# Kernel optimization log

Hardware: AMD Instinct MI355X
Metric: run time of the kernel (lower is better)

## Reference

```python
import jax, jax.numpy as jnp
import numpy as np

H = 256   # hidden size
E = 128   # embedding dim per step
C = 512   # context dim (640 - 128)
V = 32000 # vocab
T = 20
B = 128


def _lstm_seq(x_seq, h0, Wih, Whh, bih, bhh):
    """Run LSTMCell over time. NOTE: faithful to the original bug — the cell
    state passed in every step is the initial zeros (updated c is discarded)."""
    c0 = jnp.zeros_like(h0)
    xg = jnp.einsum('tbe,ge->tbg', x_seq, Wih) + bih  # precompute input gates [T,B,4H]

    def step(h, xg_t):
        g = xg_t + h @ Whh.T + bhh
        i, f, gg, o = jnp.split(g, 4, axis=-1)
        c_new = jax.nn.sigmoid(f) * c0 + jax.nn.sigmoid(i) * jnp.tanh(gg)
        h_new = jax.nn.sigmoid(o) * jnp.tanh(c_new)
        return h_new, h_new

    _, hs = jax.lax.scan(step, h0, xg)
    return hs  # [T,B,H]


def setup_inputs() -> dict:
    key = jax.random.key(0)
    ks = jax.random.split(key, 16)
    s = 0.05
    inp = {
        'inputPrev': jax.random.normal(ks[0], (T, B, E), jnp.float32),
        'inputNext': jax.random.normal(ks[1], (T, B, E), jnp.float32),
        'context':   jax.random.normal(ks[2], (B, C), jnp.float32),
        'hidden1':   jax.random.normal(ks[3], (1, H), jnp.float32) * s,
        'hidden2':   jax.random.normal(ks[4], (1, H), jnp.float32) * s,
        'Wih_p': jax.random.normal(ks[5], (4 * H, E + C), jnp.float32) * s,
        'Whh_p': jax.random.normal(ks[6], (4 * H, H), jnp.float32) * s,
        'bih_p': jax.random.normal(ks[7], (4 * H,), jnp.float32) * s,
        'bhh_p': jax.random.normal(ks[8], (4 * H,), jnp.float32) * s,
        'Wih_n': jax.random.normal(ks[9], (4 * H, E + C), jnp.float32) * s,
        'Whh_n': jax.random.normal(ks[10], (4 * H, H), jnp.float32) * s,
        'bih_n': jax.random.normal(ks[11], (4 * H,), jnp.float32) * s,
        'bhh_n': jax.random.normal(ks[12], (4 * H,), jnp.float32) * s,
        'Wp': jax.random.normal(ks[13], (V, H), jnp.float32) * s,
        'bp': jax.random.normal(ks[14], (V,), jnp.float32) * s,
    }
    return inp


def reference(inputPrev, inputNext, context, hidden1, hidden2,
              Wih_p, Whh_p, bih_p, bhh_p,
              Wih_n, Whh_n, bih_n, bhh_n, Wp, bp):
    ctx = jnp.broadcast_to(context, (T, B, C))
    x_prev = jnp.concatenate([inputPrev, ctx], axis=-1)  # [T,B,640]
    x_next = jnp.concatenate([inputNext, ctx], axis=-1)

    h10 = jnp.broadcast_to(hidden1, (B, H))
    h20 = jnp.broadcast_to(hidden2, (B, H))

    hs_prev = _lstm_seq(x_prev, h10, Wih_p, Whh_p, bih_p, bhh_p)  # [T,B,H]
    hs_next = _lstm_seq(x_next, h20, Wih_n, Whh_n, bih_n, bhh_n)

    logits_prev = jnp.einsum('tbh,vh->tbv', hs_prev, Wp) + bp
    logits_next = jnp.einsum('tbh,vh->tbv', hs_next, Wp) + bp
    return (logits_prev, logits_next)
```

## Files before the change

### kernel.cpp

```cpp
#include <hip/hip_runtime.h>
#include <cstdint>
#include <cstddef>

#define T_STEPS 20
#define B_SZ 128
#define H_SZ 256
#define E_SZ 128
#define C_SZ 512
#define V_SZ 32000
#define G3H 768

typedef __bf16 bf16x8 __attribute__((ext_vector_type(8)));
typedef float f32x4 __attribute__((ext_vector_type(4)));
typedef unsigned short u16x8 __attribute__((ext_vector_type(8)));

#define AS1 __attribute__((address_space(1)))
#define AS3 __attribute__((address_space(3)))

__device__ __forceinline__ unsigned short f2bf(float f) {
  unsigned int u = __builtin_bit_cast(unsigned int, f);
  u += 0x7fffu + ((u >> 16) & 1u);
  return (unsigned short)(u >> 16);
}

__global__ void k_zero(int* __restrict__ c) {
  if (threadIdx.x < 64) c[threadIdx.x] = 0;
}

__global__ __launch_bounds__(256) void k_prep(const float* __restrict__ Whh_p,
    const float* __restrict__ Whh_n, const float* __restrict__ h1, const float* __restrict__ h2,
    unsigned short* __restrict__ whh_bs, unsigned short* __restrict__ hsb) {
  const int idx = blockIdx.x * 256 + threadIdx.x;
  const int NW = 2 * 16 * 48 * 256;
  if (idx < NW) {
    const int k = idx & 255;
    const int n = (idx >> 8) % 48;
    const int tt = ((idx >> 8) / 48) & 15;
    const int l = idx / (16 * 48 * 256);
    const int gate = n >> 4;
    const int c = n & 15;
    const int row = (gate == 0 ? 0 : (gate == 1 ? 512 : 768)) + tt * 16 + c;
    const int ksrc = (k & 7) | (((k >> 3) ^ (n & 7)) << 3);
    const float* W = l ? Whh_n : Whh_p;
    whh_bs[idx] = f2bf(W[(size_t)row * 256 + ksrc]);
  } else {
    const int i2 = idx - NW;
    const int k = i2 & 255;
    const int b = (i2 >> 8) & 127;
    const int l = i2 >> 15;
    const int ksrc = (k & 7) | (((k >> 3) ^ (b & 7)) << 3);
    const float* h = l ? h2 : h1;
    hsb[(size_t)(l * 21) * 32768 + (size_t)b * 256 + k] = f2bf(h[ksrc]);
  }
}

__global__ __launch_bounds__(256) void k_ctx_gemm(const float* __restrict__ context,
    const float* __restrict__ Wih_p, const float* __restrict__ Wih_n,
    const float* __restrict__ bih_p, const float* __restrict__ bhh_p,
    const float* __restrict__ bih_n, const float* __restrict__ bhh_n,
    float* __restrict__ ctxg) {
  const int bid = blockIdx.x;
  const int l = bid / 48;
  const int bt = (bid / 3) & 15;
  const int gt = bid % 3;
  const int b0 = bt * 8;
  const int g = gt * 256 + threadIdx.x;
  const int row = g + (gt > 0 ? 256 : 0);
  __shared__ float csh[8][C_SZ];
  for (int i = threadIdx.x; i < 8 * C_SZ; i += 256)
    csh[i >> 9][i & 511] = context[(size_t)(b0 + (i >> 9)) * C_SZ + (i & 511)];
  __syncthreads();
  const float* W = (l ? Wih_n : Wih_p) + (size_t)row * 640 + E_SZ;
  float acc[8] = {};
  for (int c = 0; c < C_SZ; c += 4) {
    const float4 w = *(const float4*)(W + c);
#pragma unroll
    for (int bb = 0; bb < 8; ++bb) {
      const float4 h = *(const float4*)(&csh[bb][c]);
      acc[bb] += w.x * h.x + w.y * h.y + w.z * h.z + w.w * h.w;
    }
  }
  const float bias = l ? (bih_n[row] + bhh_n[row]) : (bih_p[row] + bhh_p[row]);
#pragma unroll
  for (int bb = 0; bb < 8; ++bb)
    ctxg[((size_t)l * B_SZ + b0 + bb) * G3H + g] = acc[bb] + bias;
}

__global__ __launch_bounds__(256) void k_in_gemm(const float* __restrict__ inP,
    const float* __restrict__ inN,
    const float* __restrict__ Wih_p, const float* __restrict__ Wih_n,
    const float* __restrict__ ctxg, float* __restrict__ xg) {
  const int bid = blockIdx.x;
  const int l = bid / 480;
  const int rest = bid % 480;
  const int rt = rest / 3;
  const int gt = rest % 3;
  const int r0 = rt * 16;
  const int g = gt * 256 + threadIdx.x;
  const int row = g + (gt > 0 ? 256 : 0);
  __shared__ float ish[16][E_SZ];
  const float* inp = l ? inN : inP;
  for (int i = threadIdx.x; i < 16 * E_SZ; i += 256)
    ish[i >> 7][i & 127] = inp[(size_t)(r0 + (i >> 7)) * E_SZ + (i & 127)];
  __syncthreads();
  const float* W = (l ? Wih_n : Wih_p) + (size_t)row * 640;
  float acc[16] = {};
  for (int k = 0; k < E_SZ; k += 4) {
    const float4 w = *(const float4*)(W + k);
#pragma unroll
    for (int rr = 0; rr < 16; ++rr) {
      const float4 h = *(const float4*)(&ish[rr][k]);
      acc[rr] += w.x * h.x + w.y * h.y + w.z * h.z + w.w * h.w;
    }
  }
#pragma unroll
  for (int rr = 0; rr < 16; ++rr) {
    const int b = (r0 + rr) & 127;
    const float cv = ctxg[((size_t)l * B_SZ + b) * G3H + g];
    xg[((size_t)l * (T_STEPS * B_SZ) + r0 + rr) * G3H + g] = acc[rr] + cv;
  }
}

__global__ __launch_bounds__(256, 1) void k_steps(const unsigned short* __restrict__ hsb_in,
    const unsigned short* __restrict__ whh_bs, const float* __restrict__ xg,
    unsigned short* __restrict__ hsb, int* __restrict__ cnt) {
  __shared__ unsigned short wls[48 * 256];
  __shared__ unsigned short hls[128 * 256];
  __shared__ float xls[128 * 3 * 16];
  const int tid = threadIdx.x;
  const int lane = tid & 63;
  const int wave = tid >> 6;
  const int l = blockIdx.x >> 4;
  const int tt = blockIdx.x & 15;

  {
    const unsigned short* wsrc = whh_bs + (size_t)(l * 16 + tt) * 12288 + tid * 8;
#pragma unroll
    for (int i = 0; i < 6; ++i)
      __builtin_amdgcn_global_load_lds((const AS1 void*)(wsrc + i * 2048),
                                       (AS3 void*)(wls + tid * 8 + i * 2048), 16, 0, 0);
  }

  for (int t = 0; t < T_STEPS; ++t) {
    const unsigned short* hsrc = hsb_in + (size_t)(l * 21 + t) * 32768 + tid * 8;
#pragma unroll
    for (int i = 0; i < 16; ++i)
      __builtin_amdgcn_global_load_lds((const AS1 void*)(hsrc + i * 2048),
                                       (AS3 void*)(hls + tid * 8 + i * 2048), 16, 0, 0);
    const size_t xgbase = ((size_t)(l * T_STEPS + t) * B_SZ) * G3H;
#pragma unroll
    for (int i = 0; i < 6; ++i) {
      const int q = tid + i * 256;
      const int b = q / 12;
      const int r = q - b * 12;
      const int gate = r >> 2;
      const int cg = r & 3;
      const float* src = xg + xgbase + (size_t)b * G3H + gate * 256 + tt * 16 + cg * 4;
      __builtin_amdgcn_global_load_lds((const AS1 void*)src,
                                       (AS3 void*)((char*)xls + q * 16), 16, 0, 0);
    }
    asm volatile("s_waitcnt vmcnt(0)" ::: "memory");
    __builtin_amdgcn_s_barrier();

    f32x4 acc[2][3] = {};
#pragma unroll
    for (int kf = 0; kf < 8; ++kf) {
      const int ch = kf * 4 + (lane >> 4);
      bf16x8 bf[3];
#pragma unroll
      for (int nt = 0; nt < 3; ++nt) {
        const int n = nt * 16 + (lane & 15);
        bf[nt] = __builtin_bit_cast(bf16x8, *(const u16x8*)(wls + n * 256 + ((ch ^ (n & 7)) << 3)));
      }
#pragma unroll
      for (int m = 0; m < 2; ++m) {
        const int b = wave * 32 + m * 16 + (lane & 15);
        const bf16x8 af = __builtin_bit_cast(bf16x8, *(const u16x8*)(hls + b * 256 + ((ch ^ (b & 7)) << 3)));
#pragma unroll
        for (int nt = 0; nt < 3; ++nt)
          acc[m][nt] = __builtin_amdgcn_mfma_f32_16x16x32_bf16(af, bf[nt], acc[m][nt], 0, 0, 0);
      }
    }

    unsigned short* hout = hsb + (size_t)(l * 21 + 1 + t) * 32768;
#pragma unroll
    for (int m = 0; m < 2; ++m) {
#pragma unroll
      for (int i = 0; i < 4; ++i) {
        const int b = wave * 32 + m * 16 + (lane >> 4) * 4 + i;
        const int col = lane & 15;
        const float gi = xls[(b * 3 + 0) * 16 + col] + acc[m][0][i];
        const float gg = xls[(b * 3 + 1) * 16 + col] + acc[m][1][i];
        const float go = xls[(b * 3 + 2) * 16 + col] + acc[m][2][i];
        const float c = (1.0f / (1.0f + expf(-gi))) * tanhf(gg);
        const float h = (1.0f / (1.0f + expf(-go))) * tanhf(c);
        const int j = tt * 16 + col;
        const int kpos = (j & 7) | (((j >> 3) ^ (b & 7)) << 3);
        hout[(size_t)b * 256 + kpos] = f2bf(h);
      }
    }

    if (t < T_STEPS - 1) {
      asm volatile("s_waitcnt vmcnt(0)" ::: "memory");
      __syncthreads();
      if (tid == 0) {
        __hip_atomic_fetch_add(&cnt[l * T_STEPS + t], 1, __ATOMIC_RELEASE, __HIP_MEMORY_SCOPE_AGENT);
        while (__hip_atomic_load(&cnt[l * T_STEPS + t], __ATOMIC_RELAXED, __HIP_MEMORY_SCOPE_AGENT) < 16)
          __builtin_amdgcn_s_sleep(1);
      }
      __syncthreads();
      __builtin_amdgcn_fence(__ATOMIC_ACQUIRE, "agent");
    }
  }
}

__global__ __launch_bounds__(256, 2) void k_proj(const unsigned short* __restrict__ hsb,
    const float* __restrict__ Wp, const float* __restrict__ bias, float* __restrict__ out) {
  __shared__ unsigned short smem[3 * 32 * 256];
  const int tid = threadIdx.x;
  const int lane = tid & 63;
  const int wave = tid >> 6;
  const int wgrp = wave >> 1;
  const int wc = wave & 1;
  const int n_base = blockIdx.x * 64 + wc * 32;
  bf16x8 bfr[2][8];
#pragma unroll
  for (int nt = 0; nt < 2; ++nt) {
    const int n_g = n_base + nt * 16 + (lane & 15);
    const float* src = Wp + (size_t)n_g * 256 + (lane >> 4) * 8;
#pragma unroll
    for (int kf = 0; kf < 8; ++kf) {
      const float4 a = *(const float4*)(src + kf * 32);
      const float4 b = *(const float4*)(src + kf * 32 + 4);
      u16x8 u;
      u[0] = f2bf(a.x); u[1] = f2bf(a.y); u[2] = f2bf(a.z); u[3] = f2bf(a.w);
      u[4] = f2bf(b.x); u[5] = f2bf(b.y); u[6] = f2bf(b.z); u[7] = f2bf(b.w);
      bfr[nt][kf] = __builtin_bit_cast(bf16x8, u);
    }
  }
  const float bv0 = bias[n_base + (lane & 15)];
  const float bv1 = bias[n_base + 16 + (lane & 15)];

#define STAGE_A(IT, BUF)                                                                   \
  {                                                                                        \
    const int it_ = (IT);                                                                  \
    const int l_ = it_ >= 80;                                                              \
    const int t_ = (it_ - l_ * 80) >> 2;                                                   \
    const int b0_ = (it_ & 3) * 32;                                                        \
    const unsigned short* src_ = hsb + (size_t)(l_ * 21 + 1 + t_) * 32768 + b0_ * 256 + tid * 8; \
    unsigned short* dst_ = smem + (BUF) * 8192 + tid * 8;                                  \
    _Pragma("unroll")                                                                      \
    for (int i_ = 0; i_ < 4; ++i_)                                                         \
      __builtin_amdgcn_global_load_lds((const AS1 void*)(src_ + i_ * 2048),                \
                                       (AS3 void*)(dst_ + i_ * 2048), 16, 0, 0);           \
  }

  STAGE_A(0, 0);
  STAGE_A(1, 1);
  const int lr = wgrp * 16 + (lane & 15);
  for (int it = 0; it < 160; ++it) {
    __builtin_amdgcn_s_barrier();
    if (it + 2 < 160) STAGE_A(it + 2, (it + 2) % 3);
    if (it == 0) { asm volatile("s_waitcnt vmcnt(8)" ::: "memory"); }
    else         { asm volatile("s_waitcnt vmcnt(16)" ::: "memory"); }
    __builtin_amdgcn_s_barrier();
    const unsigned short* sA = smem + (it % 3) * 8192;
    f32x4 acc0 = {}, acc1 = {};
#pragma unroll
    for (int kf = 0; kf < 8; ++kf) {
      const int ch = (kf * 4 + (lane >> 4)) ^ (lr & 7);
      const bf16x8 af = __builtin_bit_cast(bf16x8, *(const u16x8*)(sA + lr * 256 + (ch << 3)));
      acc0 = __builtin_amdgcn_mfma_f32_16x16x32_bf16(af, bfr[0][kf], acc0, 0, 0, 0);
      acc1 = __builtin_amdgcn_mfma_f32_16x16x32_bf16(af, bfr[1][kf], acc1, 0, 0, 0);
    }
    const size_t row0 = (size_t)it * 32 + wgrp * 16 + (lane >> 4) * 4;
    float* o0 = out + row0 * V_SZ + n_base + (lane & 15);
#pragma unroll
    for (int i = 0; i < 4; ++i) {
      __builtin_nontemporal_store(acc0[i] + bv0, &o0[(size_t)i * V_SZ]);
      __builtin_nontemporal_store(acc1[i] + bv1, &o0[(size_t)i * V_SZ + 16]);
    }
  }
#undef STAGE_A
}

extern "C" void kernel_launch(void* const* d_in, const int* in_sizes, int n_in,
                              void* d_out, int out_size, void* d_ws, size_t ws_size,
                              hipStream_t stream) {
  (void)in_sizes; (void)n_in; (void)out_size; (void)ws_size;
  const float* inputPrev = (const float*)d_in[0];
  const float* inputNext = (const float*)d_in[1];
  const float* context   = (const float*)d_in[2];
  const float* hidden1   = (const float*)d_in[3];
  const float* hidden2   = (const float*)d_in[4];
  const float* Wih_p = (const float*)d_in[5];
  const float* Whh_p = (const float*)d_in[6];
  const float* bih_p = (const float*)d_in[7];
  const float* bhh_p = (const float*)d_in[8];
  const float* Wih_n = (const float*)d_in[9];
  const float* Whh_n = (const float*)d_in[10];
  const float* bih_n = (const float*)d_in[11];
  const float* bhh_n = (const float*)d_in[12];
  const float* Wp = (const float*)d_in[13];
  const float* bp = (const float*)d_in[14];
  float* out = (float*)d_out;

  char* ws = (char*)d_ws;
  float* xg_all        = (float*)(ws + 0);
  float* ctxg          = (float*)(ws + 15728640);
  unsigned short* hsb  = (unsigned short*)(ws + 16515072);
  unsigned short* whhb = (unsigned short*)(ws + 19267584);
  int* cnt             = (int*)(ws + 20054016);

  k_zero<<<1, 64, 0, stream>>>(cnt);
  k_prep<<<1792, 256, 0, stream>>>(Whh_p, Whh_n, hidden1, hidden2, whhb, hsb);
  k_ctx_gemm<<<96, 256, 0, stream>>>(context, Wih_p, Wih_n, bih_p, bhh_p, bih_n, bhh_n, ctxg);
  k_in_gemm<<<960, 256, 0, stream>>>(inputPrev, inputNext, Wih_p, Wih_n, ctxg, xg_all);
  k_steps<<<32, 256, 0, stream>>>(hsb, whhb, xg_all, hsb, cnt);
  k_proj<<<500, 256, 0, stream>>>(hsb, Wp, bp, out);
}
```

Baseline: 372.0 us.

## Partition LSTM recurrence by batch to remove cross-block grid synchronization

The recurrent step kernel is re-partitioned so that each block owns 16 batch rows and all 768 gate columns, instead of 16 gate columns across all 128 batch rows. Each block keeps its hidden state in LDS, which removes the per-step global atomic barrier across 16 blocks and the per-step reload of the full hidden state. The cost is that the whole recurrent weight matrix is streamed from global/L2 through a double-buffered LDS pipeline every step, and only 16 blocks run. The initial hidden broadcast moves into the step kernel, and the counter-zeroing kernel is dropped.

```diff
diff --git a/kernel.cpp b/kernel.cpp
--- a/kernel.cpp
+++ b/kernel.cpp
@@ -23,35 +23,18 @@
   return (unsigned short)(u >> 16);
 }
 
-__global__ void k_zero(int* __restrict__ c) {
-  if (threadIdx.x < 64) c[threadIdx.x] = 0;
-}
-
 __global__ __launch_bounds__(256) void k_prep(const float* __restrict__ Whh_p,
-    const float* __restrict__ Whh_n, const float* __restrict__ h1, const float* __restrict__ h2,
-    unsigned short* __restrict__ whh_bs, unsigned short* __restrict__ hsb) {
+    const float* __restrict__ Whh_n, unsigned short* __restrict__ whh_bs) {
   const int idx = blockIdx.x * 256 + threadIdx.x;
-  const int NW = 2 * 16 * 48 * 256;
-  if (idx < NW) {
-    const int k = idx & 255;
-    const int n = (idx >> 8) % 48;
-    const int tt = ((idx >> 8) / 48) & 15;
-    const int l = idx / (16 * 48 * 256);
-    const int gate = n >> 4;
-    const int c = n & 15;
-    const int row = (gate == 0 ? 0 : (gate == 1 ? 512 : 768)) + tt * 16 + c;
-    const int ksrc = (k & 7) | (((k >> 3) ^ (n & 7)) << 3);
-    const float* W = l ? Whh_n : Whh_p;
-    whh_bs[idx] = f2bf(W[(size_t)row * 256 + ksrc]);
-  } else {
-    const int i2 = idx - NW;
-    const int k = i2 & 255;
-    const int b = (i2 >> 8) & 127;
-    const int l = i2 >> 15;
-    const int ksrc = (k & 7) | (((k >> 3) ^ (b & 7)) << 3);
-    const float* h = l ? h2 : h1;
-    hsb[(size_t)(l * 21) * 32768 + (size_t)b * 256 + k] = f2bf(h[ksrc]);
-  }
+  const int k = idx & 255;
+  const int r = (idx >> 8) % 768;
+  const int l = idx / (768 * 256);
+  const int gate = r >> 8;
+  const int col = r & 255;
+  const int row = (gate == 0 ? 0 : (gate == 1 ? 512 : 768)) + col;
+  const int ksrc = (k & 7) | (((k >> 3) ^ (r & 7)) << 3);
+  const float* W = l ? Whh_n : Whh_p;
+  whh_bs[idx] = f2bf(W[(size_t)row * 256 + ksrc]);
 }
 
 __global__ __launch_bounds__(256) void k_ctx_gemm(const float* __restrict__ context,
@@ -121,97 +104,109 @@
   }
 }
 
-__global__ __launch_bounds__(256, 1) void k_steps(const unsigned short* __restrict__ hsb_in,
-    const unsigned short* __restrict__ whh_bs, const float* __restrict__ xg,
-    unsigned short* __restrict__ hsb, int* __restrict__ cnt) {
-  __shared__ unsigned short wls[48 * 256];
-  __shared__ unsigned short hls[128 * 256];
-  __shared__ float xls[128 * 3 * 16];
+__global__ __launch_bounds__(256, 1) void k_steps(const unsigned short* __restrict__ whh_bs,
+    const float* __restrict__ xg, const float* __restrict__ h1, const float* __restrict__ h2,
+    unsigned short* __restrict__ hsb) {
+  __shared__ unsigned short buf[2][64 * 256];
+  __shared__ unsigned short hls[16 * 256];
   const int tid = threadIdx.x;
   const int lane = tid & 63;
   const int wave = tid >> 6;
-  const int l = blockIdx.x >> 4;
-  const int tt = blockIdx.x & 15;
+  const int l = blockIdx.x >> 3;
+  const int bt = blockIdx.x & 7;
 
   {
-    const unsigned short* wsrc = whh_bs + (size_t)(l * 16 + tt) * 12288 + tid * 8;
-#pragma unroll
-    for (int i = 0; i < 6; ++i)
-      __builtin_amdgcn_global_load_lds((const AS1 void*)(wsrc + i * 2048),
-                                       (AS3 void*)(wls + tid * 8 + i * 2048), 16, 0, 0);
+    const float* h0src = l ? h2 : h1;
+    const unsigned short hb = f2bf(h0src[tid]);
+    const int klo = tid & 7, khi = tid >> 3;
+#pragma unroll
+    for (int b = 0; b < 16; ++b)
+      hls[b * 256 + ((((khi) ^ (b & 7)) << 3) | klo)] = hb;
+  }
+  __syncthreads();
+
+  const unsigned short* wbase = whh_bs + (size_t)l * 768 * 256;
+  const int jn = wave * 16 + (lane & 15);
+  const int bloc = (lane >> 4) * 4;
+
+#define STAGE_W(C, BUF)                                                                  \
+  {                                                                                      \
+    const unsigned short* src_ = wbase + (size_t)(C) * 64 * 256 + tid * 8;               \
+    unsigned short* dst_ = (unsigned short*)buf[(BUF)] + tid * 8;                        \
+    _Pragma("unroll")                                                                    \
+    for (int i_ = 0; i_ < 8; ++i_)                                                       \
+      __builtin_amdgcn_global_load_lds((const AS1 void*)(src_ + i_ * 2048),              \
+                                       (AS3 void*)(dst_ + i_ * 2048), 16, 0, 0);         \
   }
 
   for (int t = 0; t < T_STEPS; ++t) {
-    const unsigned short* hsrc = hsb_in + (size_t)(l * 21 + t) * 32768 + tid * 8;
-#pragma unroll
-    for (int i = 0; i < 16; ++i)
-      __builtin_amdgcn_global_load_lds((const AS1 void*)(hsrc + i * 2048),
-                                       (AS3 void*)(hls + tid * 8 + i * 2048), 16, 0, 0);
-    const size_t xgbase = ((size_t)(l * T_STEPS + t) * B_SZ) * G3H;
-#pragma unroll
-    for (int i = 0; i < 6; ++i) {
-      const int q = tid + i * 256;
-      const int b = q / 12;
-      const int r = q - b * 12;
-      const int gate = r >> 2;
-      const int cg = r & 3;
-      const float* src = xg + xgbase + (size_t)b * G3H + gate * 256 + tt * 16 + cg * 4;
-      __builtin_amdgcn_global_load_lds((const AS1 void*)src,
-                                       (AS3 void*)((char*)xls + q * 16), 16, 0, 0);
-    }
-    asm volatile("s_waitcnt vmcnt(0)" ::: "memory");
-    __builtin_amdgcn_s_barrier();
-
-    f32x4 acc[2][3] = {};
-#pragma unroll
-    for (int kf = 0; kf < 8; ++kf) {
-      const int ch = kf * 4 + (lane >> 4);
-      bf16x8 bf[3];
-#pragma unroll
-      for (int nt = 0; nt < 3; ++nt) {
-        const int n = nt * 16 + (lane & 15);
-        bf[nt] = __builtin_bit_cast(bf16x8, *(const u16x8*)(wls + n * 256 + ((ch ^ (n & 7)) << 3)));
+    float xgv[3][4][4];
+    {
+      const float* xrow = xg + ((size_t)(l * T_STEPS + t) * B_SZ + bt * 16 + bloc) * G3H;
+#pragma unroll
+      for (int gate = 0; gate < 3; ++gate)
+#pragma unroll
+        for (int cg = 0; cg < 4; ++cg)
+#pragma unroll
+          for (int ii = 0; ii < 3 + 1; ++ii)
+            xgv[gate][cg][ii] = xrow[(size_t)ii * G3H + gate * 256 + cg * 64 + jn];
+    }
+    bf16x8 af[8];
+    {
+      const int b = lane & 15;
+#pragma unroll
+      for (int kf = 0; kf < 8; ++kf) {
+        const int ch = kf * 4 + (lane >> 4);
+        af[kf] = __builtin_bit_cast(bf16x8, *(const u16x8*)(hls + b * 256 + ((ch ^ (b & 7)) << 3)));
       }
-#pragma unroll
-      for (int m = 0; m < 2; ++m) {
-        const int b = wave * 32 + m * 16 + (lane & 15);
-        const bf16x8 af = __builtin_bit_cast(bf16x8, *(const u16x8*)(hls + b * 256 + ((ch ^ (b & 7)) << 3)));
-#pragma unroll
-        for (int nt = 0; nt < 3; ++nt)
-          acc[m][nt] = __builtin_amdgcn_mfma_f32_16x16x32_bf16(af, bf[nt], acc[m][nt], 0, 0, 0);
+    }
+
+    f32x4 acc[12];
+#pragma unroll
+    for (int c = 0; c < 12; ++c) acc[c] = f32x4{0.f, 0.f, 0.f, 0.f};
+
+    STAGE_W(0, 0);
+#pragma unroll
+    for (int c = 0; c < 12; ++c) {
+      if (c < 11) {
+        STAGE_W(c + 1, (c + 1) & 1);
+        asm volatile("s_waitcnt vmcnt(8)" ::: "memory");
+      } else {
+        asm volatile("s_waitcnt vmcnt(0)" ::: "memory");
       }
-    }
-
-    unsigned short* hout = hsb + (size_t)(l * 21 + 1 + t) * 32768;
-#pragma unroll
-    for (int m = 0; m < 2; ++m) {
-#pragma unroll
-      for (int i = 0; i < 4; ++i) {
-        const int b = wave * 32 + m * 16 + (lane >> 4) * 4 + i;
-        const int col = lane & 15;
-        const float gi = xls[(b * 3 + 0) * 16 + col] + acc[m][0][i];
-        const float gg = xls[(b * 3 + 1) * 16 + col] + acc[m][1][i];
-        const float go = xls[(b * 3 + 2) * 16 + col] + acc[m][2][i];
-        const float c = (1.0f / (1.0f + expf(-gi))) * tanhf(gg);
-        const float h = (1.0f / (1.0f + expf(-go))) * tanhf(c);
-        const int j = tt * 16 + col;
+      __builtin_amdgcn_s_barrier();
+      const unsigned short* wb = (const unsigned short*)buf[c & 1];
+#pragma unroll
+      for (int kf = 0; kf < 8; ++kf) {
+        const int ch = kf * 4 + (lane >> 4);
+        const bf16x8 bfv = __builtin_bit_cast(bf16x8,
+            *(const u16x8*)(wb + jn * 256 + ((ch ^ (jn & 7)) << 3)));
+        acc[c] = __builtin_amdgcn_mfma_f32_16x16x32_bf16(af[kf], bfv, acc[c], 0, 0, 0);
+      }
+      __builtin_amdgcn_s_barrier();
+    }
+
+    unsigned short* hout = hsb + (size_t)(l * T_STEPS + t) * 32768;
+#pragma unroll
+    for (int cg = 0; cg < 4; ++cg) {
+      const int j = cg * 64 + jn;
+#pragma unroll
+      for (int ii = 0; ii < 4; ++ii) {
+        const int b = bloc + ii;
+        const float gi = xgv[0][cg][ii] + acc[cg][ii];
+        const float gg = xgv[1][cg][ii] + acc[4 + cg][ii];
+        const float go = xgv[2][cg][ii] + acc[8 + cg][ii];
+        const float cc = (1.0f / (1.0f + expf(-gi))) * tanhf(gg);
+        const float h = (1.0f / (1.0f + expf(-go))) * tanhf(cc);
+        const unsigned short hb = f2bf(h);
         const int kpos = (j & 7) | (((j >> 3) ^ (b & 7)) << 3);
-        hout[(size_t)b * 256 + kpos] = f2bf(h);
+        hout[(size_t)(bt * 16 + b) * 256 + kpos] = hb;
+        hls[b * 256 + kpos] = hb;
       }
     }
-
-    if (t < T_STEPS - 1) {
-      asm volatile("s_waitcnt vmcnt(0)" ::: "memory");
-      __syncthreads();
-      if (tid == 0) {
-        __hip_atomic_fetch_add(&cnt[l * T_STEPS + t], 1, __ATOMIC_RELEASE, __HIP_MEMORY_SCOPE_AGENT);
-        while (__hip_atomic_load(&cnt[l * T_STEPS + t], __ATOMIC_RELAXED, __HIP_MEMORY_SCOPE_AGENT) < 16)
-          __builtin_amdgcn_s_sleep(1);
-      }
-      __syncthreads();
-      __builtin_amdgcn_fence(__ATOMIC_ACQUIRE, "agent");
-    }
-  }
+    __syncthreads();
+  }
+#undef STAGE_W
 }
 
 __global__ __launch_bounds__(256, 2) void k_proj(const unsigned short* __restrict__ hsb,
@@ -247,7 +242,7 @@
     const int l_ = it_ >= 80;                                                              \
     const int t_ = (it_ - l_ * 80) >> 2;                                                   \
     const int b0_ = (it_ & 3) * 32;                                                        \
-    const unsigned short* src_ = hsb + (size_t)(l_ * 21 + 1 + t_) * 32768 + b0_ * 256 + tid * 8; \
+    const unsigned short* src_ = hsb + (size_t)(l_ * T_STEPS + t_) * 32768 + b0_ * 256 + tid * 8; \
     unsigned short* dst_ = smem + (BUF) * 8192 + tid * 8;                                  \
     _Pragma("unroll")                                                                      \
     for (int i_ = 0; i_ < 4; ++i_)                                                         \
@@ -309,13 +304,11 @@
   float* xg_all        = (float*)(ws + 0);
   float* ctxg          = (float*)(ws + 15728640);
   unsigned short* hsb  = (unsigned short*)(ws + 16515072);
-  unsigned short* whhb = (unsigned short*)(ws + 19267584);
-  int* cnt             = (int*)(ws + 20054016);
-
-  k_zero<<<1, 64, 0, stream>>>(cnt);
-  k_prep<<<1792, 256, 0, stream>>>(Whh_p, Whh_n, hidden1, hidden2, whhb, hsb);
+  unsigned short* whhb = (unsigned short*)(ws + 19136512);
+
+  k_prep<<<1536, 256, 0, stream>>>(Whh_p, Whh_n, whhb);
   k_ctx_gemm<<<96, 256, 0, stream>>>(context, Wih_p, Wih_n, bih_p, bhh_p, bih_n, bhh_n, ctxg);
   k_in_gemm<<<960, 256, 0, stream>>>(inputPrev, inputNext, Wih_p, Wih_n, ctxg, xg_all);
-  k_steps<<<32, 256, 0, stream>>>(hsb, whhb, xg_all, hsb, cnt);
+  k_steps<<<16, 256, 0, stream>>>(whhb, xg_all, hidden1, hidden2, hsb);
   k_proj<<<500, 256, 0, stream>>>(hsb, Wp, bp, out);
 }
```

Measured after the change: 450.6 us. 1.21x slower.

## Fuse recurrent steps and vocab projection into one persistent kernel with dataflow waits

Applied to the files above, without the earlier changes.

Merges the recurrent-step kernel and the output projection into one persistent kernel of 256 blocks. The first 32 blocks run the LSTM steps and publish per-step counters. All blocks then take vocab strips from an atomic ticket queue. Before staging each hidden-state tile, the projection waits on that step's counter, so projection of early timesteps overlaps the later recurrent steps. The aim is to hide the projection behind the serial recurrence and remove a kernel launch boundary, at the cost of spin-waiting blocks, a reordered output traversal, and a dependence on all blocks being co-resident.

```diff
diff --git a/kernel.cpp b/kernel.cpp
--- a/kernel.cpp
+++ b/kernel.cpp
@@ -21,6 +21,14 @@
   unsigned int u = __builtin_bit_cast(unsigned int, f);
   u += 0x7fffu + ((u >> 16) & 1u);
   return (unsigned short)(u >> 16);
+}
+
+template <int SLEEP>
+__device__ __forceinline__ void wait16(int* p) {
+  for (int i = 0; i < 4000000; ++i) {
+    if (__hip_atomic_load(p, __ATOMIC_RELAXED, __HIP_MEMORY_SCOPE_AGENT) >= 16) return;
+    __builtin_amdgcn_s_sleep(SLEEP);
+  }
 }
 
 __global__ void k_zero(int* __restrict__ c) {
@@ -121,167 +129,184 @@
   }
 }
 
-__global__ __launch_bounds__(256, 1) void k_steps(const unsigned short* __restrict__ hsb_in,
-    const unsigned short* __restrict__ whh_bs, const float* __restrict__ xg,
-    unsigned short* __restrict__ hsb, int* __restrict__ cnt) {
-  __shared__ unsigned short wls[48 * 256];
-  __shared__ unsigned short hls[128 * 256];
-  __shared__ float xls[128 * 3 * 16];
+__global__ __launch_bounds__(256, 1) void k_mega(const unsigned short* __restrict__ whh_bs,
+    const float* __restrict__ xg, unsigned short* __restrict__ hsb,
+    const float* __restrict__ Wp, const float* __restrict__ bias, float* __restrict__ out,
+    int* __restrict__ cnt) {
+  __shared__ __align__(16) unsigned char lds[114688];
+  __shared__ int tkt_s;
   const int tid = threadIdx.x;
   const int lane = tid & 63;
   const int wave = tid >> 6;
-  const int l = blockIdx.x >> 4;
-  const int tt = blockIdx.x & 15;
-
-  {
-    const unsigned short* wsrc = whh_bs + (size_t)(l * 16 + tt) * 12288 + tid * 8;
-#pragma unroll
-    for (int i = 0; i < 6; ++i)
-      __builtin_amdgcn_global_load_lds((const AS1 void*)(wsrc + i * 2048),
-                                       (AS3 void*)(wls + tid * 8 + i * 2048), 16, 0, 0);
-  }
-
-  for (int t = 0; t < T_STEPS; ++t) {
-    const unsigned short* hsrc = hsb_in + (size_t)(l * 21 + t) * 32768 + tid * 8;
-#pragma unroll
-    for (int i = 0; i < 16; ++i)
-      __builtin_amdgcn_global_load_lds((const AS1 void*)(hsrc + i * 2048),
-                                       (AS3 void*)(hls + tid * 8 + i * 2048), 16, 0, 0);
-    const size_t xgbase = ((size_t)(l * T_STEPS + t) * B_SZ) * G3H;
-#pragma unroll
-    for (int i = 0; i < 6; ++i) {
-      const int q = tid + i * 256;
-      const int b = q / 12;
-      const int r = q - b * 12;
-      const int gate = r >> 2;
-      const int cg = r & 3;
-      const float* src = xg + xgbase + (size_t)b * G3H + gate * 256 + tt * 16 + cg * 4;
-      __builtin_amdgcn_global_load_lds((const AS1 void*)src,
-                                       (AS3 void*)((char*)xls + q * 16), 16, 0, 0);
-    }
-    asm volatile("s_waitcnt vmcnt(0)" ::: "memory");
-    __builtin_amdgcn_s_barrier();
-
-    f32x4 acc[2][3] = {};
-#pragma unroll
-    for (int kf = 0; kf < 8; ++kf) {
-      const int ch = kf * 4 + (lane >> 4);
-      bf16x8 bf[3];
-#pragma unroll
-      for (int nt = 0; nt < 3; ++nt) {
-        const int n = nt * 16 + (lane & 15);
-        bf[nt] = __builtin_bit_cast(bf16x8, *(const u16x8*)(wls + n * 256 + ((ch ^ (n & 7)) << 3)));
-      }
+
+  if (blockIdx.x < 32) {
+    unsigned short* wls = (unsigned short*)lds;
+    unsigned short* hls = (unsigned short*)(lds + 24576);
+    float* xls = (float*)(lds + 90112);
+    const int l = blockIdx.x >> 4;
+    const int tt = blockIdx.x & 15;
+    {
+      const unsigned short* wsrc = whh_bs + (size_t)(l * 16 + tt) * 12288 + tid * 8;
+#pragma unroll
+      for (int i = 0; i < 6; ++i)
+        __builtin_amdgcn_global_load_lds((const AS1 void*)(wsrc + i * 2048),
+                                         (AS3 void*)(wls + tid * 8 + i * 2048), 16, 0, 0);
+    }
+    for (int t = 0; t < T_STEPS; ++t) {
+      const unsigned short* hsrc = hsb + (size_t)(l * 21 + t) * 32768 + tid * 8;
+#pragma unroll
+      for (int i = 0; i < 16; ++i)
+        __builtin_amdgcn_global_load_lds((const AS1 void*)(hsrc + i * 2048),
+                                         (AS3 void*)(hls + tid * 8 + i * 2048), 16, 0, 0);
+      const size_t xgbase = ((size_t)(l * T_STEPS + t) * B_SZ) * G3H;
+#pragma unroll
+      for (int i = 0; i < 6; ++i) {
+        const int q = tid + i * 256;
+        const int b = q / 12;
+        const int r = q - b * 12;
+        const int gate = r >> 2;
+        const int cg = r & 3;
+        const float* src = xg + xgbase + (size_t)b * G3H + gate * 256 + tt * 16 + cg * 4;
+        __builtin_amdgcn_global_load_lds((const AS1 void*)src,
+                                         (AS3 void*)((char*)xls + q * 16), 16, 0, 0);
+      }
+      asm volatile("s_waitcnt vmcnt(0)" ::: "memory");
+      __builtin_amdgcn_s_barrier();
+
+      f32x4 acc[2][3] = {};
+#pragma unroll
+      for (int kf = 0; kf < 8; ++kf) {
+        const int ch = kf * 4 + (lane >> 4);
+        bf16x8 bf[3];
+#pragma unroll
+        for (int nt = 0; nt < 3; ++nt) {
+          const int n = nt * 16 + (lane & 15);
+          bf[nt] = __builtin_bit_cast(bf16x8, *(const u16x8*)(wls + n * 256 + ((ch ^ (n & 7)) << 3)));
+        }
+#pragma unroll
+        for (int m = 0; m < 2; ++m) {
+          const int b = wave * 32 + m * 16 + (lane & 15);
+          const bf16x8 af = __builtin_bit_cast(bf16x8, *(const u16x8*)(hls + b * 256 + ((ch ^ (b & 7)) << 3)));
+#pragma unroll
+          for (int nt = 0; nt < 3; ++nt)
+            acc[m][nt] = __builtin_amdgcn_mfma_f32_16x16x32_bf16(af, bf[nt], acc[m][nt], 0, 0, 0);
+        }
+      }
+
+      unsigned short* hout = hsb + (size_t)(l * 21 + 1 + t) * 32768;
 #pragma unroll
       for (int m = 0; m < 2; ++m) {
-        const int b = wave * 32 + m * 16 + (lane & 15);
-        const bf16x8 af = __builtin_bit_cast(bf16x8, *(const u16x8*)(hls + b * 256 + ((ch ^ (b & 7)) << 3)));
-#pragma unroll
-        for (int nt = 0; nt < 3; ++nt)
-          acc[m][nt] = __builtin_amdgcn_mfma_f32_16x16x32_bf16(af, bf[nt], acc[m][nt], 0, 0, 0);
-      }
-    }
-
-    unsigned short* hout = hsb + (size_t)(l * 21 + 1 + t) * 32768;
-#pragma unroll
-    for (int m = 0; m < 2; ++m) {
-#pragma unroll
-      for (int i = 0; i < 4; ++i) {
-        const int b = wave * 32 + m * 16 + (lane >> 4) * 4 + i;
-        const int col = lane & 15;
-        const float gi = xls[(b * 3 + 0) * 16 + col] + acc[m][0][i];
-        const float gg = xls[(b * 3 + 1) * 16 + col] + acc[m][1][i];
-        const float go = xls[(b * 3 + 2) * 16 + col] + acc[m][2][i];
-        const float c = (1.0f / (1.0f + expf(-gi))) * tanhf(gg);
-        const float h = (1.0f / (1.0f + expf(-go))) * tanhf(c);
-        const int j = tt * 16 + col;
-        const int kpos = (j & 7) | (((j >> 3) ^ (b & 7)) << 3);
-        hout[(size_t)b * 256 + kpos] = f2bf(h);
-      }
-    }
-
-    if (t < T_STEPS - 1) {
+#pragma unroll
+        for (int i = 0; i < 4; ++i) {
+          const int b = wave * 32 + m * 16 + (lane >> 4) * 4 + i;
+          const int col = lane & 15;
+          const float gi = xls[(b * 3 + 0) * 16 + col] + acc[m][0][i];
+          const float gg = xls[(b * 3 + 1) * 16 + col] + acc[m][1][i];
+          const float go = xls[(b * 3 + 2) * 16 + col] + acc[m][2][i];
+          const float cc = (1.0f / (1.0f + expf(-gi))) * tanhf(gg);
+          const float h = (1.0f / (1.0f + expf(-go))) * tanhf(cc);
+          const int jc = tt * 16 + col;
+          const int kpos = (jc & 7) | (((jc >> 3) ^ (b & 7)) << 3);
+          hout[(size_t)b * 256 + kpos] = f2bf(h);
+        }
+      }
+
       asm volatile("s_waitcnt vmcnt(0)" ::: "memory");
       __syncthreads();
-      if (tid == 0) {
+      if (tid == 0)
         __hip_atomic_fetch_add(&cnt[l * T_STEPS + t], 1, __ATOMIC_RELEASE, __HIP_MEMORY_SCOPE_AGENT);
-        while (__hip_atomic_load(&cnt[l * T_STEPS + t], __ATOMIC_RELAXED, __HIP_MEMORY_SCOPE_AGENT) < 16)
-          __builtin_amdgcn_s_sleep(1);
-      }
-      __syncthreads();
-      __builtin_amdgcn_fence(__ATOMIC_ACQUIRE, "agent");
-    }
-  }
-}
-
-__global__ __launch_bounds__(256, 2) void k_proj(const unsigned short* __restrict__ hsb,
-    const float* __restrict__ Wp, const float* __restrict__ bias, float* __restrict__ out) {
-  __shared__ unsigned short smem[3 * 32 * 256];
-  const int tid = threadIdx.x;
-  const int lane = tid & 63;
-  const int wave = tid >> 6;
+      if (t < T_STEPS - 1) {
+        if (tid == 0) wait16<1>(&cnt[l * T_STEPS + t]);
+        __syncthreads();
+        __builtin_amdgcn_fence(__ATOMIC_ACQUIRE, "agent");
+      }
+    }
+  }
+
+  unsigned short* smem = (unsigned short*)lds;
   const int wgrp = wave >> 1;
   const int wc = wave & 1;
-  const int n_base = blockIdx.x * 64 + wc * 32;
-  bf16x8 bfr[2][8];
-#pragma unroll
-  for (int nt = 0; nt < 2; ++nt) {
-    const int n_g = n_base + nt * 16 + (lane & 15);
-    const float* src = Wp + (size_t)n_g * 256 + (lane >> 4) * 8;
-#pragma unroll
-    for (int kf = 0; kf < 8; ++kf) {
-      const float4 a = *(const float4*)(src + kf * 32);
-      const float4 b = *(const float4*)(src + kf * 32 + 4);
-      u16x8 u;
-      u[0] = f2bf(a.x); u[1] = f2bf(a.y); u[2] = f2bf(a.z); u[3] = f2bf(a.w);
-      u[4] = f2bf(b.x); u[5] = f2bf(b.y); u[6] = f2bf(b.z); u[7] = f2bf(b.w);
-      bfr[nt][kf] = __builtin_bit_cast(bf16x8, u);
-    }
-  }
-  const float bv0 = bias[n_base + (lane & 15)];
-  const float bv1 = bias[n_base + 16 + (lane & 15)];
-
-#define STAGE_A(IT, BUF)                                                                   \
-  {                                                                                        \
-    const int it_ = (IT);                                                                  \
-    const int l_ = it_ >= 80;                                                              \
-    const int t_ = (it_ - l_ * 80) >> 2;                                                   \
-    const int b0_ = (it_ & 3) * 32;                                                        \
-    const unsigned short* src_ = hsb + (size_t)(l_ * 21 + 1 + t_) * 32768 + b0_ * 256 + tid * 8; \
-    unsigned short* dst_ = smem + (BUF) * 8192 + tid * 8;                                  \
-    _Pragma("unroll")                                                                      \
-    for (int i_ = 0; i_ < 4; ++i_)                                                         \
-      __builtin_amdgcn_global_load_lds((const AS1 void*)(src_ + i_ * 2048),                \
-                                       (AS3 void*)(dst_ + i_ * 2048), 16, 0, 0);           \
-  }
-
-  STAGE_A(0, 0);
-  STAGE_A(1, 1);
   const int lr = wgrp * 16 + (lane & 15);
-  for (int it = 0; it < 160; ++it) {
-    __builtin_amdgcn_s_barrier();
-    if (it + 2 < 160) STAGE_A(it + 2, (it + 2) % 3);
-    if (it == 0) { asm volatile("s_waitcnt vmcnt(8)" ::: "memory"); }
-    else         { asm volatile("s_waitcnt vmcnt(16)" ::: "memory"); }
-    __builtin_amdgcn_s_barrier();
-    const unsigned short* sA = smem + (it % 3) * 8192;
-    f32x4 acc0 = {}, acc1 = {};
-#pragma unroll
-    for (int kf = 0; kf < 8; ++kf) {
-      const int ch = (kf * 4 + (lane >> 4)) ^ (lr & 7);
-      const bf16x8 af = __builtin_bit_cast(bf16x8, *(const u16x8*)(sA + lr * 256 + (ch << 3)));
-      acc0 = __builtin_amdgcn_mfma_f32_16x16x32_bf16(af, bfr[0][kf], acc0, 0, 0, 0);
-      acc1 = __builtin_amdgcn_mfma_f32_16x16x32_bf16(af, bfr[1][kf], acc1, 0, 0, 0);
-    }
-    const size_t row0 = (size_t)it * 32 + wgrp * 16 + (lane >> 4) * 4;
-    float* o0 = out + row0 * V_SZ + n_base + (lane & 15);
-#pragma unroll
-    for (int i = 0; i < 4; ++i) {
-      __builtin_nontemporal_store(acc0[i] + bv0, &o0[(size_t)i * V_SZ]);
-      __builtin_nontemporal_store(acc1[i] + bv1, &o0[(size_t)i * V_SZ + 16]);
-    }
-  }
+  int seen0 = -1, seen1 = -1;
+
+  for (;;) {
+    __syncthreads();
+    if (tid == 0)
+      tkt_s = __hip_atomic_fetch_add(&cnt[63], 1, __ATOMIC_RELAXED, __HIP_MEMORY_SCOPE_AGENT);
+    __syncthreads();
+    const int strip = tkt_s;
+    if (strip >= 500) break;
+    const int n_base = strip * 64 + wc * 32;
+
+    bf16x8 bfr[2][8];
+#pragma unroll
+    for (int nt = 0; nt < 2; ++nt) {
+      const int n_g = n_base + nt * 16 + (lane & 15);
+      const float* src = Wp + (size_t)n_g * 256 + (lane >> 4) * 8;
+#pragma unroll
+      for (int kf = 0; kf < 8; ++kf) {
+        const float4 a = *(const float4*)(src + kf * 32);
+        const float4 b = *(const float4*)(src + kf * 32 + 4);
+        u16x8 u;
+        u[0] = f2bf(a.x); u[1] = f2bf(a.y); u[2] = f2bf(a.z); u[3] = f2bf(a.w);
+        u[4] = f2bf(b.x); u[5] = f2bf(b.y); u[6] = f2bf(b.z); u[7] = f2bf(b.w);
+        bfr[nt][kf] = __builtin_bit_cast(bf16x8, u);
+      }
+    }
+    const float bv0 = bias[n_base + (lane & 15)];
+    const float bv1 = bias[n_base + 16 + (lane & 15)];
+
+#define ENSURE(J)                                                                          \
+    {                                                                                      \
+      const int t_ = (J) >> 3, l_ = ((J) >> 2) & 1;                                        \
+      int& s_ = l_ ? seen1 : seen0;                                                        \
+      if (t_ > s_) {                                                                       \
+        wait16<16>(&cnt[l_ * T_STEPS + t_]);                                               \
+        __builtin_amdgcn_fence(__ATOMIC_ACQUIRE, "agent");                                 \
+        s_ = t_;                                                                           \
+      }                                                                                    \
+    }
+#define STAGE_A(J, BUF)                                                                    \
+    {                                                                                      \
+      const int t_ = (J) >> 3, l_ = ((J) >> 2) & 1, q_ = (J) & 3;                          \
+      const unsigned short* src_ = hsb + (size_t)(l_ * 21 + 1 + t_) * 32768 + q_ * 8192 + tid * 8; \
+      unsigned short* dst_ = smem + (BUF) * 8192 + tid * 8;                                \
+      _Pragma("unroll")                                                                    \
+      for (int i_ = 0; i_ < 4; ++i_)                                                       \
+        __builtin_amdgcn_global_load_lds((const AS1 void*)(src_ + i_ * 2048),              \
+                                         (AS3 void*)(dst_ + i_ * 2048), 16, 0, 0);         \
+    }
+
+    ENSURE(0); STAGE_A(0, 0);
+    ENSURE(1); STAGE_A(1, 1);
+    for (int j = 0; j < 160; ++j) {
+      __builtin_amdgcn_s_barrier();
+      if (j + 2 < 160) { ENSURE(j + 2); STAGE_A(j + 2, (j + 2) % 3); }
+      if (j == 0) { asm volatile("s_waitcnt vmcnt(8)" ::: "memory"); }
+      else        { asm volatile("s_waitcnt vmcnt(16)" ::: "memory"); }
+      __builtin_amdgcn_s_barrier();
+      const unsigned short* sA = smem + (j % 3) * 8192;
+      f32x4 acc0 = {}, acc1 = {};
+#pragma unroll
+      for (int kf = 0; kf < 8; ++kf) {
+        const int ch = (kf * 4 + (lane >> 4)) ^ (lr & 7);
+        const bf16x8 af = __builtin_bit_cast(bf16x8, *(const u16x8*)(sA + lr * 256 + (ch << 3)));
+        acc0 = __builtin_amdgcn_mfma_f32_16x16x32_bf16(af, bfr[0][kf], acc0, 0, 0, 0);
+        acc1 = __builtin_amdgcn_mfma_f32_16x16x32_bf16(af, bfr[1][kf], acc1, 0, 0, 0);
+      }
+      const int t_ = j >> 3, l_ = (j >> 2) & 1, q_ = j & 3;
+      const int it = l_ * 80 + t_ * 4 + q_;
+      const size_t row0 = (size_t)it * 32 + wgrp * 16 + (lane >> 4) * 4;
+      float* o0 = out + row0 * V_SZ + n_base + (lane & 15);
+#pragma unroll
+      for (int i = 0; i < 4; ++i) {
+        __builtin_nontemporal_store(acc0[i] + bv0, &o0[(size_t)i * V_SZ]);
+        __builtin_nontemporal_store(acc1[i] + bv1, &o0[(size_t)i * V_SZ + 16]);
+      }
+    }
+#undef ENSURE
 #undef STAGE_A
+  }
 }
 
 extern "C" void kernel_launch(void* const* d_in, const int* in_sizes, int n_in,
@@ -316,6 +341,5 @@
   k_prep<<<1792, 256, 0, stream>>>(Whh_p, Whh_n, hidden1, hidden2, whhb, hsb);
   k_ctx_gemm<<<96, 256, 0, stream>>>(context, Wih_p, Wih_n, bih_p, bhh_p, bih_n, bhh_n, ctxg);
   k_in_gemm<<<960, 256, 0, stream>>>(inputPrev, inputNext, Wih_p, Wih_n, ctxg, xg_all);
-  k_steps<<<32, 256, 0, stream>>>(hsb, whhb, xg_all, hsb, cnt);
-  k_proj<<<500, 256, 0, stream>>>(hsb, Wp, bp, out);
-}
+  k_mega<<<256, 256, 0, stream>>>(whhb, xg_all, hsb, Wp, bp, out, cnt);
+}
```

Result: slower. 668.7 us (+79.7%).
